# Kernel optimization log

Measured on AMD Instinct MI355X. Metric: run time of the kernel, lower is better.

## Reference

```python
import jax, jax.numpy as jnp
import numpy as np

N_QUBITS = 10
N_LAYERS = 4
BATCH = 4096


def _apply_1q_batched(state, gate, q):
    # state: [B, 2,2,...,2]; gate: [B, 2, 2] (per-sample angles)
    s = jnp.moveaxis(state, 1 + q, -1)
    s = jnp.einsum('b...i,bji->b...j', s, gate)
    return jnp.moveaxis(s, -1, 1 + q)


def _apply_1q(state, gate, q):
    # gate: [2, 2] shared across batch
    s = jnp.moveaxis(state, 1 + q, -1)
    s = jnp.einsum('b...i,ji->b...j', s, gate)
    return jnp.moveaxis(s, -1, 1 + q)


def _apply_cnot(state, c, t):
    # bring control axis to 1 and target axis to 2, flip target where control==1
    s = jnp.moveaxis(state, (1 + c, 1 + t), (1, 2))
    s = jnp.concatenate([s[:, :1], s[:, 1:, ::-1]], axis=1)
    return jnp.moveaxis(s, (1, 2), (1 + c, 1 + t))


def _ry_rz_gate(theta_y, theta_z):
    # RZ(theta_z) @ RY(theta_y), both scalars -> [2, 2] complex
    hy = theta_y * 0.5
    cy, sy = jnp.cos(hy), jnp.sin(hy)
    ry = jnp.stack([jnp.stack([cy, -sy]), jnp.stack([sy, cy])]).astype(jnp.complex64)
    hz = theta_z * 0.5
    ph = jnp.exp(1j * jnp.stack([-hz, hz]).astype(jnp.complex64))  # diag of RZ
    return ph[:, None] * ry


def setup_inputs() -> dict:
    key = jax.random.key(0)
    kx, kp = jax.random.split(key)
    x = jax.random.uniform(kx, (BATCH, N_QUBITS), dtype=jnp.float32,
                           minval=-np.pi, maxval=np.pi)
    params = 0.5 * jax.random.normal(kp, (N_LAYERS, 2 * N_QUBITS), dtype=jnp.float32)
    return {"x": x, "params": params}


def reference(x, params):
    B, n = x.shape
    L = params.shape[0]
    dim = 2 ** n
    # |0...0> for every sample
    state = jnp.zeros((B, dim), jnp.complex64).at[:, 0].set(1.0)
    state = state.reshape((B,) + (2,) * n)

    # data encoding: RY(x[b, q]) on qubit q, per-sample angles
    half = x * 0.5
    c, s = jnp.cos(half), jnp.sin(half)  # [B, n]
    for q in range(n):
        g = jnp.stack([jnp.stack([c[:, q], -s[:, q]], -1),
                       jnp.stack([s[:, q], c[:, q]], -1)], -2).astype(jnp.complex64)  # [B,2,2]
        state = _apply_1q_batched(state, g, q)

    # variational layers: RY then RZ (fused) per qubit, then CNOT ring
    for l in range(L):
        for q in range(n):
            state = _apply_1q(state, _ry_rz_gate(params[l, q], params[l, n + q]), q)
        for q in range(n):
            state = _apply_cnot(state, q, (q + 1) % n)

    # <Z_q> = sum over basis states of |amp|^2 * (+1 if bit_q==0 else -1)
    probs = jnp.abs(state.reshape(B, dim)) ** 2  # float32 [B, 2^n]
    idx = jnp.arange(dim)
    bits = (idx[None, :] >> (n - 1 - jnp.arange(n))[:, None]) & 1  # [n, 2^n]
    signs = (1.0 - 2.0 * bits).astype(probs.dtype)
    return jnp.einsum('bs,qs->bq', probs, signs)  # [B, n]
```

## Files before the change

### kernel.cpp

```cpp
#include <hip/hip_runtime.h>

#define NQ 10

typedef float v2f __attribute__((ext_vector_type(2)));

struct M10 { unsigned r[10]; };

constexpr M10 mk_R() {
    M10 A{};
    A.r[0] = 0b1111111110u;
    for (int k = 1; k < 10; ++k) A.r[k] = (1u << (k + 1)) - 1u;
    return A;
}
constexpr M10 mk_Rinv() {
    M10 A{};
    A.r[0] = (1u << 0) | (1u << 9);
    A.r[1] = (1u << 0) | (1u << 1) | (1u << 9);
    for (int k = 2; k < 10; ++k) A.r[k] = (1u << (k - 1)) | (1u << k);
    return A;
}
constexpr M10 mmul(M10 A, M10 B) {
    M10 C{};
    for (int k = 0; k < 10; ++k) {
        unsigned v = 0;
        for (int j = 0; j < 10; ++j)
            if ((A.r[k] >> j) & 1u) v ^= B.r[j];
        C.r[k] = v;
    }
    return C;
}
constexpr M10 RF  = mk_R();
constexpr M10 RV  = mk_Rinv();
constexpr M10 RF2 = mmul(RF, RF);
constexpr M10 RF3 = mmul(RF2, RF);
constexpr M10 RF4 = mmul(RF2, RF2);
constexpr M10 RV2 = mmul(RV, RV);
constexpr M10 RV3 = mmul(RV2, RV);

constexpr bool isI(M10 A) {
    for (int k = 0; k < 10; ++k) if (A.r[k] != (1u << k)) return false;
    return true;
}
static_assert(isI(mmul(RF, RV)), "Rinv wrong");
static_assert(isI(mmul(RV3, RF3)), "powers wrong");

constexpr unsigned colq(M10 A, int q) {
    unsigned m = 0;
    for (int k = 0; k < 10; ++k) m |= ((A.r[k] >> q) & 1u) << k;
    return m;
}
constexpr int laneM(unsigned qm) {
    int m = 0;
    for (int q = 0; q <= 5; ++q) if ((qm >> q) & 1u) m |= 1 << (5 - q);
    return m;
}
constexpr int regM(unsigned qm) {
    int m = 0;
    for (int q = 6; q <= 9; ++q) if ((qm >> q) & 1u) m |= 1 << (9 - q);
    return m;
}

template<int CTRL>
__device__ __forceinline__ float dppmov(float v) {
    return __int_as_float(__builtin_amdgcn_mov_dpp(__float_as_int(v), CTRL, 0xF, 0xF, true));
}
template<int M>
__device__ __forceinline__ float lx(float v) {
    static_assert(M > 0 && M < 64, "mask");
    if constexpr (M == 1)       return dppmov<0xB1>(v);
    else if constexpr (M == 2)  return dppmov<0x4E>(v);
    else if constexpr (M == 3)  return dppmov<0x1B>(v);
    else if constexpr (M == 7)  return dppmov<0x141>(v);
    else if constexpr (M == 8)  return dppmov<0x128>(v);
    else if constexpr (M == 15) return dppmov<0x140>(v);
    else if constexpr (M == 4)  return lx<3>(lx<7>(v));
    else if constexpr (M == 5)  return lx<2>(lx<7>(v));
    else if constexpr (M == 6)  return lx<1>(lx<7>(v));
    else if constexpr (M == 9)  return lx<1>(lx<8>(v));
    else if constexpr (M == 10) return lx<2>(lx<8>(v));
    else if constexpr (M == 11) return lx<3>(lx<8>(v));
    else if constexpr (M == 12) return lx<3>(lx<15>(v));
    else if constexpr (M == 13) return lx<2>(lx<15>(v));
    else if constexpr (M == 14) return lx<1>(lx<15>(v));
    else if constexpr (M < 32)
        return __int_as_float(__builtin_amdgcn_ds_swizzle(__float_as_int(v), (M << 10) | 0x1F));
    else
        return __shfl_xor(v, M, 64);
}

__device__ __forceinline__ v2f cmul(v2f a, v2f b) {
    v2f n; n.x = -a.y; n.y = a.y;
    return a.xx * b + n * b.yx;
}

template<int LM, int RM, int LW, int RW>
__device__ __forceinline__ void ry_g(v2f st[16], int lane, float c, float s) {
    static_assert((LM | RM) != 0, "null mask");
    const float baseP = (__builtin_popcount((unsigned)(lane & LW)) & 1) ? s : -s;
    if constexpr (RM == 0) {
#pragma unroll
        for (int r = 0; r < 16; ++r) {
            v2f part;
            part.x = lx<LM ? LM : 1>(st[r].x);
            part.y = lx<LM ? LM : 1>(st[r].y);
            const float cB = (__builtin_popcount((unsigned)(r & RW)) & 1) ? -baseP : baseP;
            st[r] = c * st[r] + cB * part;
        }
    } else {
        constexpr int PIV = RM & (-RM);
#pragma unroll
        for (int r = 0; r < 16; ++r) {
            if (r & PIV) continue;
            const int rb = r ^ RM;
            v2f ea, eb;
            if constexpr (LM != 0) {
                ea.x = lx<LM ? LM : 1>(st[r].x);  ea.y = lx<LM ? LM : 1>(st[r].y);
                eb.x = lx<LM ? LM : 1>(st[rb].x); eb.y = lx<LM ? LM : 1>(st[rb].y);
            } else {
                ea = st[r]; eb = st[rb];
            }
            const float cBa = (__builtin_popcount((unsigned)(r & RW)) & 1) ? -baseP : baseP;
            const float cBb = (__builtin_popcount((unsigned)(rb & RW)) & 1) ? -baseP : baseP;
            st[r]  = c * st[r]  + cBa * eb;
            st[rb] = c * st[rb] + cBb * ea;
        }
    }
}

template<int L>
__device__ __forceinline__ void diag_g(v2f st[16], int lane, const float* pl) {
    constexpr M10 W = (L == 1) ? RF : RF2;
    float G[16];
#pragma unroll
    for (int i = 0; i < 16; ++i) G[i] = 0.f;
#pragma unroll
    for (int q = 0; q < 10; ++q) {
        const int LWq = laneM(W.r[q]);
        const int RWq = regM(W.r[q]);
        const float hz = 0.5f * pl[10 + q];
        const float gq = (__builtin_popcount((unsigned)(lane & LWq)) & 1) ? hz : -hz;
        G[RWq] += gq;
    }
#pragma unroll
    for (int m = 1; m < 16; m <<= 1) {
#pragma unroll
        for (int r = 0; r < 16; ++r) {
            if (r & m) continue;
            const float a = G[r], bb = G[r | m];
            G[r] = a + bb;
            G[r | m] = a - bb;
        }
    }
#pragma unroll
    for (int r = 0; r < 16; ++r) {
        float sn, cs;
        __sincosf(G[r], &sn, &cs);
        v2f d; d.x = cs; d.y = sn;
        st[r] = cmul(st[r], d);
    }
}

__device__ __forceinline__ float wht64(float v, int lane) {
    float t;
    t = lx<1>(v);  v = (lane & 1)  ? (t - v) : (v + t);
    t = lx<2>(v);  v = (lane & 2)  ? (t - v) : (v + t);
    t = lx<4>(v);  v = (lane & 4)  ? (t - v) : (v + t);
    t = lx<8>(v);  v = (lane & 8)  ? (t - v) : (v + t);
    t = lx<16>(v); v = (lane & 16) ? (t - v) : (v + t);
    t = lx<32>(v); v = (lane & 32) ? (t - v) : (v + t);
    return v;
}

__global__ __launch_bounds__(256)
void pqc_kernel(const float* __restrict__ x,
                const float* __restrict__ params,
                float* __restrict__ out, int B) {
    const int lane = threadIdx.x & 63;
    const int wave = threadIdx.x >> 6;
    const int b = blockIdx.x * 4 + wave;
    if (b >= B) return;

    const float* xb = x + (long)b * NQ;
    const float* p0 = params;
    float a0,b0,a1,b1,a2,b2,a3,b3,a4,b4,a5,b5,a6,b6,a7,b7,a8,b8,a9,b9;
    float cz0,sz0,cz1,sz1,cz2,sz2,cz3,sz3,cz4,sz4,cz5,sz5,cz6,sz6,cz7,sz7,cz8,sz8,cz9,sz9;
    __sincosf(0.5f * (xb[0] + p0[0]), &b0, &a0);
    __sincosf(0.5f * (xb[1] + p0[1]), &b1, &a1);
    __sincosf(0.5f * (xb[2] + p0[2]), &b2, &a2);
    __sincosf(0.5f * (xb[3] + p0[3]), &b3, &a3);
    __sincosf(0.5f * (xb[4] + p0[4]), &b4, &a4);
    __sincosf(0.5f * (xb[5] + p0[5]), &b5, &a5);
    __sincosf(0.5f * (xb[6] + p0[6]), &b6, &a6);
    __sincosf(0.5f * (xb[7] + p0[7]), &b7, &a7);
    __sincosf(0.5f * (xb[8] + p0[8]), &b8, &a8);
    __sincosf(0.5f * (xb[9] + p0[9]), &b9, &a9);
    __sincosf(0.5f * p0[10], &sz0, &cz0);
    __sincosf(0.5f * p0[11], &sz1, &cz1);
    __sincosf(0.5f * p0[12], &sz2, &cz2);
    __sincosf(0.5f * p0[13], &sz3, &cz3);
    __sincosf(0.5f * p0[14], &sz4, &cz4);
    __sincosf(0.5f * p0[15], &sz5, &cz5);
    __sincosf(0.5f * p0[16], &sz6, &cz6);
    __sincosf(0.5f * p0[17], &sz7, &cz7);
    __sincosf(0.5f * p0[18], &sz8, &cz8);
    __sincosf(0.5f * p0[19], &sz9, &cz9);

    float R = ((lane & 32) ? b0 : a0) * ((lane & 16) ? b1 : a1)
            * ((lane & 8)  ? b2 : a2) * ((lane & 4)  ? b3 : a3)
            * ((lane & 2)  ? b4 : a4) * ((lane & 1)  ? b5 : a5);
    v2f P; P.x = cz0; P.y = (lane & 32) ? sz0 : -sz0;
    { v2f t; t.x = cz1; t.y = (lane & 16) ? sz1 : -sz1; P = cmul(P, t); }
    { v2f t; t.x = cz2; t.y = (lane & 8)  ? sz2 : -sz2; P = cmul(P, t); }
    { v2f t; t.x = cz3; t.y = (lane & 4)  ? sz3 : -sz3; P = cmul(P, t); }
    { v2f t; t.x = cz4; t.y = (lane & 2)  ? sz4 : -sz4; P = cmul(P, t); }
    { v2f t; t.x = cz5; t.y = (lane & 1)  ? sz5 : -sz5; P = cmul(P, t); }
    v2f laneC = R * P;

    v2f u6l = { a6 * cz6, -a6 * sz6 }, u6h = { b6 * cz6, b6 * sz6 };
    v2f u7l = { a7 * cz7, -a7 * sz7 }, u7h = { b7 * cz7, b7 * sz7 };
    v2f u8l = { a8 * cz8, -a8 * sz8 }, u8h = { b8 * cz8, b8 * sz8 };
    v2f u9l = { a9 * cz9, -a9 * sz9 }, u9h = { b9 * cz9, b9 * sz9 };
    v2f A2[4] = { cmul(u6l, u7l), cmul(u6l, u7h), cmul(u6h, u7l), cmul(u6h, u7h) };
    v2f B2[4] = { cmul(u8l, u9l), cmul(u8l, u9h), cmul(u8h, u9l), cmul(u8h, u9h) };
    v2f LA[4] = { cmul(laneC, A2[0]), cmul(laneC, A2[1]),
                  cmul(laneC, A2[2]), cmul(laneC, A2[3]) };

    v2f st[16];
#pragma unroll
    for (int r = 0; r < 16; ++r) st[r] = cmul(LA[r >> 2], B2[r & 3]);

#define GATE(INV, ROLE, Q, ANG) do { \
    float gc_, gs_; __sincosf(0.5f * (ANG), &gs_, &gc_); \
    ry_g<laneM(colq(INV, Q)), regM(colq(INV, Q)), \
         laneM(ROLE.r[Q]), regM(ROLE.r[Q])>(st, lane, gc_, gs_); \
} while (0)

    {
        const float* pl = params + 20;
        GATE(RV, RF, 0, pl[0]); GATE(RV, RF, 1, pl[1]);
        GATE(RV, RF, 2, pl[2]); GATE(RV, RF, 3, pl[3]);
        GATE(RV, RF, 4, pl[4]); GATE(RV, RF, 5, pl[5]);
        GATE(RV, RF, 6, pl[6]); GATE(RV, RF, 7, pl[7]);
        GATE(RV, RF, 8, pl[8]); GATE(RV, RF, 9, pl[9]);
        diag_g<1>(st, lane, pl);
    }
    {
        const float* pl = params + 40;
        GATE(RV2, RF2, 0, pl[0]); GATE(RV2, RF2, 1, pl[1]);
        GATE(RV2, RF2, 2, pl[2]); GATE(RV2, RF2, 3, pl[3]);
        GATE(RV2, RF2, 4, pl[4]); GATE(RV2, RF2, 5, pl[5]);
        GATE(RV2, RF2, 6, pl[6]); GATE(RV2, RF2, 7, pl[7]);
        GATE(RV2, RF2, 8, pl[8]); GATE(RV2, RF2, 9, pl[9]);
        diag_g<2>(st, lane, pl);
    }
    {
        const float* pl = params + 60;
        GATE(RV3, RF3, 0, pl[0]); GATE(RV3, RF3, 1, pl[1]);
        GATE(RV3, RF3, 2, pl[2]); GATE(RV3, RF3, 3, pl[3]);
        GATE(RV3, RF3, 4, pl[4]); GATE(RV3, RF3, 5, pl[5]);
        GATE(RV3, RF3, 6, pl[6]); GATE(RV3, RF3, 7, pl[7]);
        GATE(RV3, RF3, 8, pl[8]); GATE(RV3, RF3, 9, pl[9]);
    }
#undef GATE

    float p[16];
#pragma unroll
    for (int r = 0; r < 16; ++r)
        p[r] = st[r].x * st[r].x + st[r].y * st[r].y;
#pragma unroll
    for (int m = 1; m < 16; m <<= 1) {
#pragma unroll
        for (int r = 0; r < 16; ++r) {
            if (r & m) continue;
            const float a = p[r], bb = p[r | m];
            p[r] = a + bb;
            p[r | m] = a - bb;
        }
    }
    const long base = (long)b * NQ;
#pragma unroll
    for (int q = 0; q < 10; ++q) {
        const int LWq = laneM(RF4.r[q]);
        const int RWq = regM(RF4.r[q]);
        const float v = wht64(p[RWq], lane);
        if (lane == LWq) out[base + q] = v;
    }
}

extern "C" void kernel_launch(void* const* d_in, const int* in_sizes, int n_in,
                              void* d_out, int out_size, void* d_ws, size_t ws_size,
                              hipStream_t stream) {
    const float* x = (const float*)d_in[0];
    const float* params = (const float*)d_in[1];
    float* out = (float*)d_out;
    const int B = in_sizes[0] / NQ;
    const int grid = (B + 3) / 4;
    pqc_kernel<<<grid, 256, 0, stream>>>(x, params, out, B);
}
```

Before: 77.85 us.

## Process two batch samples per wavefront to share gate setup and interleave shuffles

Each wavefront now simulates two samples, holding two 16-register state arrays, so gate angle sincos, the RZ phase table and per-lane coefficients are computed once for both. Processing the two states side by side gives independent shuffle and FMA chains that can hide cross-lane latency. The cost is doubled register pressure, which may lower occupancy (launch bounds now ask for 2 blocks), and half as many blocks in the grid. There is no bounds check for the second sample, so an odd batch size would write out of range.

```diff
diff --git a/kernel.cpp b/kernel.cpp
--- a/kernel.cpp
+++ b/kernel.cpp
@@ -94,17 +94,18 @@
 }
 
 template<int LM, int RM, int LW, int RW>
-__device__ __forceinline__ void ry_g(v2f st[16], int lane, float c, float s) {
+__device__ __forceinline__ void ry_g2(v2f sa[16], v2f sb[16], int lane, float c, float s) {
     static_assert((LM | RM) != 0, "null mask");
     const float baseP = (__builtin_popcount((unsigned)(lane & LW)) & 1) ? s : -s;
     if constexpr (RM == 0) {
 #pragma unroll
         for (int r = 0; r < 16; ++r) {
-            v2f part;
-            part.x = lx<LM ? LM : 1>(st[r].x);
-            part.y = lx<LM ? LM : 1>(st[r].y);
+            v2f pa, pb;
+            pa.x = lx<LM ? LM : 1>(sa[r].x); pa.y = lx<LM ? LM : 1>(sa[r].y);
+            pb.x = lx<LM ? LM : 1>(sb[r].x); pb.y = lx<LM ? LM : 1>(sb[r].y);
             const float cB = (__builtin_popcount((unsigned)(r & RW)) & 1) ? -baseP : baseP;
-            st[r] = c * st[r] + cB * part;
+            sa[r] = c * sa[r] + cB * pa;
+            sb[r] = c * sb[r] + cB * pb;
         }
     } else {
         constexpr int PIV = RM & (-RM);
@@ -112,23 +113,27 @@
         for (int r = 0; r < 16; ++r) {
             if (r & PIV) continue;
             const int rb = r ^ RM;
-            v2f ea, eb;
+            v2f eaA, ebA, eaB, ebB;
             if constexpr (LM != 0) {
-                ea.x = lx<LM ? LM : 1>(st[r].x);  ea.y = lx<LM ? LM : 1>(st[r].y);
-                eb.x = lx<LM ? LM : 1>(st[rb].x); eb.y = lx<LM ? LM : 1>(st[rb].y);
+                eaA.x = lx<LM ? LM : 1>(sa[r].x);  eaA.y = lx<LM ? LM : 1>(sa[r].y);
+                ebA.x = lx<LM ? LM : 1>(sa[rb].x); ebA.y = lx<LM ? LM : 1>(sa[rb].y);
+                eaB.x = lx<LM ? LM : 1>(sb[r].x);  eaB.y = lx<LM ? LM : 1>(sb[r].y);
+                ebB.x = lx<LM ? LM : 1>(sb[rb].x); ebB.y = lx<LM ? LM : 1>(sb[rb].y);
             } else {
-                ea = st[r]; eb = st[rb];
+                eaA = sa[r]; ebA = sa[rb]; eaB = sb[r]; ebB = sb[rb];
             }
             const float cBa = (__builtin_popcount((unsigned)(r & RW)) & 1) ? -baseP : baseP;
             const float cBb = (__builtin_popcount((unsigned)(rb & RW)) & 1) ? -baseP : baseP;
-            st[r]  = c * st[r]  + cBa * eb;
-            st[rb] = c * st[rb] + cBb * ea;
+            sa[r]  = c * sa[r]  + cBa * ebA;
+            sa[rb] = c * sa[rb] + cBb * eaA;
+            sb[r]  = c * sb[r]  + cBa * ebB;
+            sb[rb] = c * sb[rb] + cBb * eaB;
         }
     }
 }
 
 template<int L>
-__device__ __forceinline__ void diag_g(v2f st[16], int lane, const float* pl) {
+__device__ __forceinline__ void diag_g2(v2f sa[16], v2f sb[16], int lane, const float* pl) {
     constexpr M10 W = (L == 1) ? RF : RF2;
     float G[16];
 #pragma unroll
@@ -156,7 +161,8 @@
         float sn, cs;
         __sincosf(G[r], &sn, &cs);
         v2f d; d.x = cs; d.y = sn;
-        st[r] = cmul(st[r], d);
+        sa[r] = cmul(sa[r], d);
+        sb[r] = cmul(sb[r], d);
     }
 }
 
@@ -171,68 +177,66 @@
     return v;
 }
 
-__global__ __launch_bounds__(256)
+__device__ __forceinline__ void encode_state(const float* xb, const float* p0,
+                                             const float* czt, const float* szt,
+                                             int lane, v2f st[16]) {
+    float a[10], bb[10];
+#pragma unroll
+    for (int q = 0; q < 10; ++q)
+        __sincosf(0.5f * (xb[q] + p0[q]), &bb[q], &a[q]);
+
+    float R = 1.f;
+    v2f P; P.x = 1.f; P.y = 0.f;
+#pragma unroll
+    for (int q = 0; q <= 5; ++q) {
+        const int m = 1 << (5 - q);
+        R *= (lane & m) ? bb[q] : a[q];
+        v2f t; t.x = czt[q]; t.y = (lane & m) ? szt[q] : -szt[q];
+        P = cmul(P, t);
+    }
+    v2f laneC = R * P;
+
+    v2f u[4][2];
+#pragma unroll
+    for (int q = 6; q <= 9; ++q) {
+        u[q - 6][0].x = a[q] * czt[q];  u[q - 6][0].y = -a[q] * szt[q];
+        u[q - 6][1].x = bb[q] * czt[q]; u[q - 6][1].y =  bb[q] * szt[q];
+    }
+    v2f A2[4], B2[4];
+#pragma unroll
+    for (int k = 0; k < 4; ++k) {
+        A2[k] = cmul(u[0][k >> 1], u[1][k & 1]);
+        B2[k] = cmul(u[2][k >> 1], u[3][k & 1]);
+    }
+    v2f LA[4] = { cmul(laneC, A2[0]), cmul(laneC, A2[1]),
+                  cmul(laneC, A2[2]), cmul(laneC, A2[3]) };
+#pragma unroll
+    for (int r = 0; r < 16; ++r) st[r] = cmul(LA[r >> 2], B2[r & 3]);
+}
+
+__global__ __launch_bounds__(256, 2)
 void pqc_kernel(const float* __restrict__ x,
                 const float* __restrict__ params,
                 float* __restrict__ out, int B) {
     const int lane = threadIdx.x & 63;
-    const int wave = threadIdx.x >> 6;
-    const int b = blockIdx.x * 4 + wave;
-    if (b >= B) return;
-
-    const float* xb = x + (long)b * NQ;
+    const int wid = threadIdx.x >> 6;
+    const int b0 = blockIdx.x * 8 + wid * 2;
+    if (b0 >= B) return;
+
     const float* p0 = params;
-    float a0,b0,a1,b1,a2,b2,a3,b3,a4,b4,a5,b5,a6,b6,a7,b7,a8,b8,a9,b9;
-    float cz0,sz0,cz1,sz1,cz2,sz2,cz3,sz3,cz4,sz4,cz5,sz5,cz6,sz6,cz7,sz7,cz8,sz8,cz9,sz9;
-    __sincosf(0.5f * (xb[0] + p0[0]), &b0, &a0);
-    __sincosf(0.5f * (xb[1] + p0[1]), &b1, &a1);
-    __sincosf(0.5f * (xb[2] + p0[2]), &b2, &a2);
-    __sincosf(0.5f * (xb[3] + p0[3]), &b3, &a3);
-    __sincosf(0.5f * (xb[4] + p0[4]), &b4, &a4);
-    __sincosf(0.5f * (xb[5] + p0[5]), &b5, &a5);
-    __sincosf(0.5f * (xb[6] + p0[6]), &b6, &a6);
-    __sincosf(0.5f * (xb[7] + p0[7]), &b7, &a7);
-    __sincosf(0.5f * (xb[8] + p0[8]), &b8, &a8);
-    __sincosf(0.5f * (xb[9] + p0[9]), &b9, &a9);
-    __sincosf(0.5f * p0[10], &sz0, &cz0);
-    __sincosf(0.5f * p0[11], &sz1, &cz1);
-    __sincosf(0.5f * p0[12], &sz2, &cz2);
-    __sincosf(0.5f * p0[13], &sz3, &cz3);
-    __sincosf(0.5f * p0[14], &sz4, &cz4);
-    __sincosf(0.5f * p0[15], &sz5, &cz5);
-    __sincosf(0.5f * p0[16], &sz6, &cz6);
-    __sincosf(0.5f * p0[17], &sz7, &cz7);
-    __sincosf(0.5f * p0[18], &sz8, &cz8);
-    __sincosf(0.5f * p0[19], &sz9, &cz9);
-
-    float R = ((lane & 32) ? b0 : a0) * ((lane & 16) ? b1 : a1)
-            * ((lane & 8)  ? b2 : a2) * ((lane & 4)  ? b3 : a3)
-            * ((lane & 2)  ? b4 : a4) * ((lane & 1)  ? b5 : a5);
-    v2f P; P.x = cz0; P.y = (lane & 32) ? sz0 : -sz0;
-    { v2f t; t.x = cz1; t.y = (lane & 16) ? sz1 : -sz1; P = cmul(P, t); }
-    { v2f t; t.x = cz2; t.y = (lane & 8)  ? sz2 : -sz2; P = cmul(P, t); }
-    { v2f t; t.x = cz3; t.y = (lane & 4)  ? sz3 : -sz3; P = cmul(P, t); }
-    { v2f t; t.x = cz4; t.y = (lane & 2)  ? sz4 : -sz4; P = cmul(P, t); }
-    { v2f t; t.x = cz5; t.y = (lane & 1)  ? sz5 : -sz5; P = cmul(P, t); }
-    v2f laneC = R * P;
-
-    v2f u6l = { a6 * cz6, -a6 * sz6 }, u6h = { b6 * cz6, b6 * sz6 };
-    v2f u7l = { a7 * cz7, -a7 * sz7 }, u7h = { b7 * cz7, b7 * sz7 };
-    v2f u8l = { a8 * cz8, -a8 * sz8 }, u8h = { b8 * cz8, b8 * sz8 };
-    v2f u9l = { a9 * cz9, -a9 * sz9 }, u9h = { b9 * cz9, b9 * sz9 };
-    v2f A2[4] = { cmul(u6l, u7l), cmul(u6l, u7h), cmul(u6h, u7l), cmul(u6h, u7h) };
-    v2f B2[4] = { cmul(u8l, u9l), cmul(u8l, u9h), cmul(u8h, u9l), cmul(u8h, u9h) };
-    v2f LA[4] = { cmul(laneC, A2[0]), cmul(laneC, A2[1]),
-                  cmul(laneC, A2[2]), cmul(laneC, A2[3]) };
-
-    v2f st[16];
-#pragma unroll
-    for (int r = 0; r < 16; ++r) st[r] = cmul(LA[r >> 2], B2[r & 3]);
+    float czt[10], szt[10];
+#pragma unroll
+    for (int q = 0; q < 10; ++q)
+        __sincosf(0.5f * p0[10 + q], &szt[q], &czt[q]);
+
+    v2f sa[16], sb[16];
+    encode_state(x + (long)b0 * NQ, p0, czt, szt, lane, sa);
+    encode_state(x + (long)(b0 + 1) * NQ, p0, czt, szt, lane, sb);
 
 #define GATE(INV, ROLE, Q, ANG) do { \
     float gc_, gs_; __sincosf(0.5f * (ANG), &gs_, &gc_); \
-    ry_g<laneM(colq(INV, Q)), regM(colq(INV, Q)), \
-         laneM(ROLE.r[Q]), regM(ROLE.r[Q])>(st, lane, gc_, gs_); \
+    ry_g2<laneM(colq(INV, Q)), regM(colq(INV, Q)), \
+          laneM(ROLE.r[Q]), regM(ROLE.r[Q])>(sa, sb, lane, gc_, gs_); \
 } while (0)
 
     {
@@ -242,7 +246,7 @@
         GATE(RV, RF, 4, pl[4]); GATE(RV, RF, 5, pl[5]);
         GATE(RV, RF, 6, pl[6]); GATE(RV, RF, 7, pl[7]);
         GATE(RV, RF, 8, pl[8]); GATE(RV, RF, 9, pl[9]);
-        diag_g<1>(st, lane, pl);
+        diag_g2<1>(sa, sb, lane, pl);
     }
     {
         const float* pl = params + 40;
@@ -251,7 +255,7 @@
         GATE(RV2, RF2, 4, pl[4]); GATE(RV2, RF2, 5, pl[5]);
         GATE(RV2, RF2, 6, pl[6]); GATE(RV2, RF2, 7, pl[7]);
         GATE(RV2, RF2, 8, pl[8]); GATE(RV2, RF2, 9, pl[9]);
-        diag_g<2>(st, lane, pl);
+        diag_g2<2>(sa, sb, lane, pl);
     }
     {
         const float* pl = params + 60;
@@ -263,27 +267,35 @@
     }
 #undef GATE
 
-    float p[16];
-#pragma unroll
-    for (int r = 0; r < 16; ++r)
-        p[r] = st[r].x * st[r].x + st[r].y * st[r].y;
+    float pA[16], pB[16];
+#pragma unroll
+    for (int r = 0; r < 16; ++r) {
+        pA[r] = sa[r].x * sa[r].x + sa[r].y * sa[r].y;
+        pB[r] = sb[r].x * sb[r].x + sb[r].y * sb[r].y;
+    }
 #pragma unroll
     for (int m = 1; m < 16; m <<= 1) {
 #pragma unroll
         for (int r = 0; r < 16; ++r) {
             if (r & m) continue;
-            const float a = p[r], bb = p[r | m];
-            p[r] = a + bb;
-            p[r | m] = a - bb;
-        }
-    }
-    const long base = (long)b * NQ;
+            const float a1 = pA[r], b1 = pA[r | m];
+            pA[r] = a1 + b1; pA[r | m] = a1 - b1;
+            const float a2 = pB[r], b2 = pB[r | m];
+            pB[r] = a2 + b2; pB[r | m] = a2 - b2;
+        }
+    }
+    const long baseA = (long)b0 * NQ;
+    const long baseB = (long)(b0 + 1) * NQ;
 #pragma unroll
     for (int q = 0; q < 10; ++q) {
         const int LWq = laneM(RF4.r[q]);
         const int RWq = regM(RF4.r[q]);
-        const float v = wht64(p[RWq], lane);
-        if (lane == LWq) out[base + q] = v;
+        const float vA = wht64(pA[RWq], lane);
+        const float vB = wht64(pB[RWq], lane);
+        if (lane == LWq) {
+            out[baseA + q] = vA;
+            out[baseB + q] = vB;
+        }
     }
 }
 
@@ -294,6 +306,6 @@
     const float* params = (const float*)d_in[1];
     float* out = (float*)d_out;
     const int B = in_sizes[0] / NQ;
-    const int grid = (B + 3) / 4;
+    const int grid = (B + 7) / 8;
     pqc_kernel<<<grid, 256, 0, stream>>>(x, params, out, B);
 }
```

After: 77.58 us. No clear change (-0.3%).
